# Kernel tuning notes

Measured on AMD Instinct MI355X. Metric: run time of the kernel, lower is better.

## Reference

```python
import jax, jax.numpy as jnp
import numpy as np


def setup_inputs() -> dict:
    key = jax.random.key(0)
    ks = jax.random.split(key, 4)
    T, B, I, H, L = 512, 64, 1024, 1024, 2
    s = 1.0 / np.sqrt(H)
    return {
        "x": jax.random.normal(ks[0], (T, B, I), dtype=jnp.float32),
        "W_ih": jax.random.uniform(ks[1], (L, 4 * H, I), dtype=jnp.float32, minval=-s, maxval=s),
        "W_hh": jax.random.uniform(ks[2], (L, 4 * H, H), dtype=jnp.float32, minval=-s, maxval=s),
        "b": jnp.zeros((L, 4 * H), dtype=jnp.float32),
        "h0": jnp.zeros((L, B, H), dtype=jnp.float32),
        "c0": jnp.zeros((L, B, H), dtype=jnp.float32),
    }


def _run_layer(xs, Wih, Whh, b, h0, c0):
    """xs: [T,B,I]; returns outputs [T,B,H], (h_T, c_T).
    Standard LSTM cell, PyTorch gate order (i, f, g, o)."""
    H = h0.shape[-1]

    # Precompute input projections for all timesteps in one big GEMM.
    gx = jnp.einsum("tbi,gi->tbg", xs, Wih) + b  # [T,B,4H]

    def step(carry, gx_t):
        h, c = carry
        g = gx_t + h @ Whh.T  # [B,4H]
        i = jax.nn.sigmoid(g[:, 0 * H:1 * H])
        f = jax.nn.sigmoid(g[:, 1 * H:2 * H])
        gg = jnp.tanh(g[:, 2 * H:3 * H])
        o = jax.nn.sigmoid(g[:, 3 * H:4 * H])
        c_next = f * c + i * gg
        h_next = o * jnp.tanh(c_next)
        return (h_next, c_next), h_next

    (h_n, c_n), out = jax.lax.scan(step, (h0, c0), gx)
    return out, h_n, c_n


def reference(x, W_ih, W_hh, b, h0, c0):
    """Eval-mode stacked LSTM (dropout=0, wdrop=0, gumbel noise p=0 -> identity).
    Returns (output [T,B,H], h_n [L,B,H], c_n [L,B,H])."""
    L = W_ih.shape[0]
    hs, cs = [], []
    layer_in = x
    for layer in range(L):
        layer_in, h_n, c_n = _run_layer(layer_in, W_ih[layer], W_hh[layer],
                                         b[layer], h0[layer], c0[layer])
        hs.append(h_n)
        cs.append(c_n)
    return layer_in, jnp.stack(hs, 0), jnp.stack(cs, 0)
```

## Files before the change

### kernel.cpp

```cpp
#include <hip/hip_runtime.h>

#define TT 512
#define BH 65536
#define NBLK 256

typedef unsigned short u16;
typedef __attribute__((ext_vector_type(8))) __bf16 bf16x8;
typedef __attribute__((ext_vector_type(4))) float f32x4;
typedef __attribute__((ext_vector_type(4))) float float4_t;
typedef __attribute__((ext_vector_type(2))) unsigned long long u64x2;

#define WS_XBF   0ull
#define WS_H1    67108864ull
#define WS_H2    (WS_H1 + 262144ull)
#define WS_FLAGS (WS_H2 + 262144ull)
#define WS_REL   (WS_FLAGS + 32768ull)

#define LDS_BYTES 132096

__device__ __forceinline__ u16 f2bf(float f) {
  unsigned u = __builtin_bit_cast(unsigned, f);
  u += 0x7fffu + ((u >> 16) & 1u);
  return (u16)(u >> 16);
}

__device__ __forceinline__ float sigm(float x) { return 1.0f / (1.0f + __expf(-x)); }
__device__ __forceinline__ float tanh_fast(float x) { return 1.0f - 2.0f / (__expf(2.0f * x) + 1.0f); }

__device__ __forceinline__ bf16x8 ld8_sc1(const u16* p) {
  u64x2 v;
  v.x = __hip_atomic_load((const unsigned long long*)p,       __ATOMIC_RELAXED, __HIP_MEMORY_SCOPE_AGENT);
  v.y = __hip_atomic_load((const unsigned long long*)(p + 4), __ATOMIC_RELAXED, __HIP_MEMORY_SCOPE_AGENT);
  return __builtin_bit_cast(bf16x8, v);
}

__global__ __launch_bounds__(256) void cast_x_kernel(const float* __restrict__ x, u16* __restrict__ xbf) {
  unsigned i = (blockIdx.x * 256u + threadIdx.x) * 4u;
  float4_t v = *(const float4_t*)(x + i);
  unsigned p0 = (unsigned)f2bf(v.x) | ((unsigned)f2bf(v.y) << 16);
  unsigned p1 = (unsigned)f2bf(v.z) | ((unsigned)f2bf(v.w) << 16);
  uint2 p; p.x = p0; p.y = p1;
  *(uint2*)(xbf + i) = p;
}

__global__ __launch_bounds__(256) void init_kernel(const float* __restrict__ h0,
                                                   u16* __restrict__ h1s, u16* __restrict__ h2s,
                                                   int* __restrict__ flags, int* __restrict__ rel) {
  unsigned idx = blockIdx.x * 256u + threadIdx.x;
  unsigned l = idx >> 16;
  unsigned pos = idx & 65535u;
  u16* dst = (l == 0 ? h1s : h2s) + BH + pos;
  *dst = f2bf(h0[idx]);
  if (idx < 8192) flags[idx] = 0;
  if (idx == 0) rel[0] = 0;
}

__global__ __launch_bounds__(256, 1) void lstm_kernel(
    const float* __restrict__ Wih, const float* __restrict__ Whh,
    const float* __restrict__ bias, const float* __restrict__ c0,
    const u16* __restrict__ xbf,
    u16* __restrict__ h1s, u16* __restrict__ h2s,
    float* __restrict__ out, int* __restrict__ flags, int* __restrict__ rel)
{
  extern __shared__ __align__(16) char smem_raw[];
  u16* lw = (u16*)smem_raw;
  const int tid = threadIdx.x;
  const int bid = blockIdx.x;
  const int layer = bid >> 7;
  const int lb = bid & 127;
  const int jbase = lb * 8;

  const float* WihL = Wih + (size_t)layer * 4096 * 1024;
  const float* WhhL = Whh + (size_t)layer * 4096 * 1024;
  for (int idx = tid; idx < 8192; idx += 256) {
    int n = idx >> 8;
    int k4 = (idx & 255) * 4;
    int gate = n >> 3, jj = n & 7;
    size_t grow = (size_t)(gate * 1024 + jbase + jj) * 1024 + k4;
    float4_t a = *(const float4_t*)(WihL + grow);
    float4_t b = *(const float4_t*)(WhhL + grow);
    u16* d0 = lw + n * 1032 + k4;
    u16* d1 = lw + 33024 + n * 1032 + k4;
    d0[0] = f2bf(a.x); d0[1] = f2bf(a.y); d0[2] = f2bf(a.z); d0[3] = f2bf(a.w);
    d1[0] = f2bf(b.x); d1[1] = f2bf(b.y); d1[2] = f2bf(b.z); d1[3] = f2bf(b.w);
  }

  const int lane = tid & 63;
  const int w = tid >> 6;
  const int q = lane >> 4;
  const int ln = lane & 15;
  const int arow = w * 16 + ln;
  const int koff = q * 8;
  const int jj = ln & 7;
  const bool act = ln < 8;
  const int col = jbase + jj;
  const int mrow0 = w * 16 + q * 4;

  const float* bL = bias + layer * 4096;
  const float bn0 = bL[(ln >> 3) * 1024 + jbase + jj];
  const float bn1 = bL[(2 + (ln >> 3)) * 1024 + jbase + jj];

  float c[4];
  {
    const float* c0L = c0 + (size_t)layer * BH;
#pragma unroll
    for (int r = 0; r < 4; ++r) c[r] = c0L[(mrow0 + r) * 1024 + col];
  }

  u16* mySlot = (layer == 0) ? h1s : h2s;
  const size_t OUT_HN = (size_t)TT * BH;
  const size_t OUT_CN = OUT_HN + 2 * BH;

  const u16* bW0 = lw + ln * 1032 + koff;
  const u16* bW1 = lw + (16 + ln) * 1032 + koff;
  const u16* bH0 = bW0 + 33024;
  const u16* bH1 = bW1 + 33024;

  __syncthreads();

  for (int it = 0; it <= TT; ++it) {
    const int t = (layer == 0) ? it : (it - 1);
    if (t >= 0 && t < TT) {
      const u16* a1p = mySlot + (size_t)((t - 1) & 1) * BH + arow * 1024 + koff;

      f32x4 acc0 = {0.f, 0.f, 0.f, 0.f};
      f32x4 acc1 = {0.f, 0.f, 0.f, 0.f};
      f32x4 acc2 = {0.f, 0.f, 0.f, 0.f};
      f32x4 acc3 = {0.f, 0.f, 0.f, 0.f};

      if (layer == 0) {
        const u16* a0p = xbf + (size_t)t * BH + arow * 1024 + koff;
#pragma unroll 16
        for (int kc = 0; kc < 32; ++kc) {
          bf16x8 a  = *(const bf16x8*)(a0p + kc * 32);
          bf16x8 b0 = *(const bf16x8*)(bW0 + kc * 32);
          bf16x8 b1 = *(const bf16x8*)(bW1 + kc * 32);
          if (kc & 1) {
            acc2 = __builtin_amdgcn_mfma_f32_16x16x32_bf16(a, b0, acc2, 0, 0, 0);
            acc3 = __builtin_amdgcn_mfma_f32_16x16x32_bf16(a, b1, acc3, 0, 0, 0);
          } else {
            acc0 = __builtin_amdgcn_mfma_f32_16x16x32_bf16(a, b0, acc0, 0, 0, 0);
            acc1 = __builtin_amdgcn_mfma_f32_16x16x32_bf16(a, b1, acc1, 0, 0, 0);
          }
        }
      } else {
        const u16* a0p = h1s + (size_t)(t & 1) * BH + arow * 1024 + koff;
#pragma unroll 16
        for (int kc = 0; kc < 32; ++kc) {
          bf16x8 a  = ld8_sc1(a0p + kc * 32);
          bf16x8 b0 = *(const bf16x8*)(bW0 + kc * 32);
          bf16x8 b1 = *(const bf16x8*)(bW1 + kc * 32);
          if (kc & 1) {
            acc2 = __builtin_amdgcn_mfma_f32_16x16x32_bf16(a, b0, acc2, 0, 0, 0);
            acc3 = __builtin_amdgcn_mfma_f32_16x16x32_bf16(a, b1, acc3, 0, 0, 0);
          } else {
            acc0 = __builtin_amdgcn_mfma_f32_16x16x32_bf16(a, b0, acc0, 0, 0, 0);
            acc1 = __builtin_amdgcn_mfma_f32_16x16x32_bf16(a, b1, acc1, 0, 0, 0);
          }
        }
      }
#pragma unroll 16
      for (int kc = 0; kc < 32; ++kc) {
        bf16x8 a  = ld8_sc1(a1p + kc * 32);
        bf16x8 b0 = *(const bf16x8*)(bH0 + kc * 32);
        bf16x8 b1 = *(const bf16x8*)(bH1 + kc * 32);
        if (kc & 1) {
          acc2 = __builtin_amdgcn_mfma_f32_16x16x32_bf16(a, b0, acc2, 0, 0, 0);
          acc3 = __builtin_amdgcn_mfma_f32_16x16x32_bf16(a, b1, acc3, 0, 0, 0);
        } else {
          acc0 = __builtin_amdgcn_mfma_f32_16x16x32_bf16(a, b0, acc0, 0, 0, 0);
          acc1 = __builtin_amdgcn_mfma_f32_16x16x32_bf16(a, b1, acc1, 0, 0, 0);
        }
      }

      float g0[4], g1[4], f4[4], o4[4];
#pragma unroll
      for (int r = 0; r < 4; ++r) { g0[r] = acc0[r] + acc2[r] + bn0; g1[r] = acc1[r] + acc3[r] + bn1; }
#pragma unroll
      for (int r = 0; r < 4; ++r) { f4[r] = __shfl_down(g0[r], 8); o4[r] = __shfl_down(g1[r], 8); }

      if (act) {
        float hn[4];
#pragma unroll
        for (int r = 0; r < 4; ++r) {
          float iv = sigm(g0[r]);
          float fv = sigm(f4[r]);
          float gv = tanh_fast(g1[r]);
          float ov = sigm(o4[r]);
          c[r] = fv * c[r] + iv * gv;
          hn[r] = ov * tanh_fast(c[r]);
        }
        u16* hdst = mySlot + (size_t)(t & 1) * BH;
#pragma unroll
        for (int r = 0; r < 4; ++r)
          __hip_atomic_store(&hdst[(mrow0 + r) * 1024 + col], f2bf(hn[r]),
                             __ATOMIC_RELAXED, __HIP_MEMORY_SCOPE_AGENT);
        if (layer == 1) {
          float* od = out + (size_t)t * BH;
#pragma unroll
          for (int r = 0; r < 4; ++r) od[(mrow0 + r) * 1024 + col] = hn[r];
        }
        if (t == TT - 1) {
#pragma unroll
          for (int r = 0; r < 4; ++r) {
            out[OUT_HN + (size_t)layer * BH + (mrow0 + r) * 1024 + col] = hn[r];
            out[OUT_CN + (size_t)layer * BH + (mrow0 + r) * 1024 + col] = c[r];
          }
        }
      }
    }

    if (it < TT) {
      __syncthreads();
      if (bid == 0) {
        if (tid > 0) {
          while (__hip_atomic_load(&flags[tid * 32], __ATOMIC_RELAXED,
                                   __HIP_MEMORY_SCOPE_AGENT) < it + 1)
            __builtin_amdgcn_s_sleep(1);
        }
        __syncthreads();
        if (tid == 0)
          __hip_atomic_store(rel, it + 1, __ATOMIC_RELAXED, __HIP_MEMORY_SCOPE_AGENT);
      } else {
        if (tid == 0) {
          __hip_atomic_store(&flags[bid * 32], it + 1, __ATOMIC_RELAXED,
                             __HIP_MEMORY_SCOPE_AGENT);
          while (__hip_atomic_load(rel, __ATOMIC_RELAXED,
                                   __HIP_MEMORY_SCOPE_AGENT) < it + 1)
            __builtin_amdgcn_s_sleep(1);
        }
        __syncthreads();
      }
      __builtin_amdgcn_fence(__ATOMIC_ACQUIRE, "workgroup");
    }
  }
}

extern "C" void kernel_launch(void* const* d_in, const int* in_sizes, int n_in,
                              void* d_out, int out_size, void* d_ws, size_t ws_size,
                              hipStream_t stream) {
  const float* x    = (const float*)d_in[0];
  const float* Wih  = (const float*)d_in[1];
  const float* Whh  = (const float*)d_in[2];
  const float* bias = (const float*)d_in[3];
  const float* h0   = (const float*)d_in[4];
  const float* c0   = (const float*)d_in[5];
  float* out = (float*)d_out;
  char* ws = (char*)d_ws;
  u16* xbf  = (u16*)(ws + WS_XBF);
  u16* h1s  = (u16*)(ws + WS_H1);
  u16* h2s  = (u16*)(ws + WS_H2);
  int* flags = (int*)(ws + WS_FLAGS);
  int* rel   = (int*)(ws + WS_REL);

  hipFuncSetAttribute((const void*)lstm_kernel,
                      hipFuncAttributeMaxDynamicSharedMemorySize, LDS_BYTES);

  cast_x_kernel<<<32768, 256, 0, stream>>>(x, xbf);
  init_kernel<<<512, 256, 0, stream>>>(h0, h1s, h2s, flags, rel);
  lstm_kernel<<<NBLK, 256, LDS_BYTES, stream>>>(Wih, Whh, bias, c0, xbf, h1s, h2s,
                                                out, flags, rel);
}
```

Before: 8.831 ms.

## Replace global barrier with per-block progress counters and a layer-1 ring buffer

Removes the centralized grid-wide barrier, in which block 0 gathered flags and released everyone each step. Each block now publishes a 16-bit progress counter, and one wavefront polls all 256 counters with packed 64-bit loads before each step. Layer 0's hidden states go into a 32-slot ring buffer, so layer 0 can run up to 31 steps ahead of layer 1 instead of moving in lockstep. Layer 0 also computes its input projection before waiting, which overlaps that work with synchronization. The cost is a larger workspace and heavier polling traffic on the counters.

```diff
diff --git a/kernel.cpp b/kernel.cpp
--- a/kernel.cpp
+++ b/kernel.cpp
@@ -2,7 +2,7 @@
 
 #define TT 512
 #define BH 65536
-#define NBLK 256
+#define NSLOT 32
 
 typedef unsigned short u16;
 typedef __attribute__((ext_vector_type(8))) __bf16 bf16x8;
@@ -11,10 +11,9 @@
 typedef __attribute__((ext_vector_type(2))) unsigned long long u64x2;
 
 #define WS_XBF   0ull
-#define WS_H1    67108864ull
-#define WS_H2    (WS_H1 + 262144ull)
-#define WS_FLAGS (WS_H2 + 262144ull)
-#define WS_REL   (WS_FLAGS + 32768ull)
+#define WS_H1R   67108864ull
+#define WS_H2    (WS_H1R + (unsigned long long)NSLOT * BH * 2)
+#define WS_CNT   (WS_H2 + 262144ull)
 
 #define LDS_BYTES 132096
 
@@ -44,23 +43,22 @@
 }
 
 __global__ __launch_bounds__(256) void init_kernel(const float* __restrict__ h0,
-                                                   u16* __restrict__ h1s, u16* __restrict__ h2s,
-                                                   int* __restrict__ flags, int* __restrict__ rel) {
+                                                   u16* __restrict__ h1r, u16* __restrict__ h2s,
+                                                   u16* __restrict__ cnt) {
   unsigned idx = blockIdx.x * 256u + threadIdx.x;
   unsigned l = idx >> 16;
   unsigned pos = idx & 65535u;
-  u16* dst = (l == 0 ? h1s : h2s) + BH + pos;
+  u16* dst = (l == 0 ? (h1r + (size_t)(NSLOT - 1) * BH) : (h2s + BH)) + pos;
   *dst = f2bf(h0[idx]);
-  if (idx < 8192) flags[idx] = 0;
-  if (idx == 0) rel[0] = 0;
+  if (idx < 256) cnt[idx] = 0;
 }
 
 __global__ __launch_bounds__(256, 1) void lstm_kernel(
     const float* __restrict__ Wih, const float* __restrict__ Whh,
     const float* __restrict__ bias, const float* __restrict__ c0,
     const u16* __restrict__ xbf,
-    u16* __restrict__ h1s, u16* __restrict__ h2s,
-    float* __restrict__ out, int* __restrict__ flags, int* __restrict__ rel)
+    u16* __restrict__ h1r, u16* __restrict__ h2s,
+    float* __restrict__ out, u16* __restrict__ cnt)
 {
   extern __shared__ __align__(16) char smem_raw[];
   u16* lw = (u16*)smem_raw;
@@ -107,7 +105,6 @@
     for (int r = 0; r < 4; ++r) c[r] = c0L[(mrow0 + r) * 1024 + col];
   }
 
-  u16* mySlot = (layer == 0) ? h1s : h2s;
   const size_t OUT_HN = (size_t)TT * BH;
   const size_t OUT_CN = OUT_HN + 2 * BH;
 
@@ -116,49 +113,53 @@
   const u16* bH0 = bW0 + 33024;
   const u16* bH1 = bW1 + 33024;
 
+  const int fragoff = arow * 1024 + koff;
+
   __syncthreads();
 
-  for (int it = 0; it <= TT; ++it) {
-    const int t = (layer == 0) ? it : (it - 1);
-    if (t >= 0 && t < TT) {
-      const u16* a1p = mySlot + (size_t)((t - 1) & 1) * BH + arow * 1024 + koff;
-
-      f32x4 acc0 = {0.f, 0.f, 0.f, 0.f};
-      f32x4 acc1 = {0.f, 0.f, 0.f, 0.f};
-      f32x4 acc2 = {0.f, 0.f, 0.f, 0.f};
-      f32x4 acc3 = {0.f, 0.f, 0.f, 0.f};
-
-      if (layer == 0) {
-        const u16* a0p = xbf + (size_t)t * BH + arow * 1024 + koff;
-#pragma unroll 16
-        for (int kc = 0; kc < 32; ++kc) {
-          bf16x8 a  = *(const bf16x8*)(a0p + kc * 32);
-          bf16x8 b0 = *(const bf16x8*)(bW0 + kc * 32);
-          bf16x8 b1 = *(const bf16x8*)(bW1 + kc * 32);
-          if (kc & 1) {
-            acc2 = __builtin_amdgcn_mfma_f32_16x16x32_bf16(a, b0, acc2, 0, 0, 0);
-            acc3 = __builtin_amdgcn_mfma_f32_16x16x32_bf16(a, b1, acc3, 0, 0, 0);
-          } else {
-            acc0 = __builtin_amdgcn_mfma_f32_16x16x32_bf16(a, b0, acc0, 0, 0, 0);
-            acc1 = __builtin_amdgcn_mfma_f32_16x16x32_bf16(a, b1, acc1, 0, 0, 0);
-          }
-        }
-      } else {
-        const u16* a0p = h1s + (size_t)(t & 1) * BH + arow * 1024 + koff;
-#pragma unroll 16
-        for (int kc = 0; kc < 32; ++kc) {
-          bf16x8 a  = ld8_sc1(a0p + kc * 32);
-          bf16x8 b0 = *(const bf16x8*)(bW0 + kc * 32);
-          bf16x8 b1 = *(const bf16x8*)(bW1 + kc * 32);
-          if (kc & 1) {
-            acc2 = __builtin_amdgcn_mfma_f32_16x16x32_bf16(a, b0, acc2, 0, 0, 0);
-            acc3 = __builtin_amdgcn_mfma_f32_16x16x32_bf16(a, b1, acc3, 0, 0, 0);
-          } else {
-            acc0 = __builtin_amdgcn_mfma_f32_16x16x32_bf16(a, b0, acc0, 0, 0, 0);
-            acc1 = __builtin_amdgcn_mfma_f32_16x16x32_bf16(a, b1, acc1, 0, 0, 0);
-          }
-        }
-      }
+  for (int t = 0; t < TT; ++t) {
+    f32x4 acc0 = {0.f, 0.f, 0.f, 0.f};
+    f32x4 acc1 = {0.f, 0.f, 0.f, 0.f};
+    f32x4 acc2 = {0.f, 0.f, 0.f, 0.f};
+    f32x4 acc3 = {0.f, 0.f, 0.f, 0.f};
+
+    if (layer == 0) {
+      const u16* a0p = xbf + (size_t)t * BH + fragoff;
+#pragma unroll 16
+      for (int kc = 0; kc < 32; ++kc) {
+        bf16x8 a  = *(const bf16x8*)(a0p + kc * 32);
+        bf16x8 b0 = *(const bf16x8*)(bW0 + kc * 32);
+        bf16x8 b1 = *(const bf16x8*)(bW1 + kc * 32);
+        if (kc & 1) {
+          acc2 = __builtin_amdgcn_mfma_f32_16x16x32_bf16(a, b0, acc2, 0, 0, 0);
+          acc3 = __builtin_amdgcn_mfma_f32_16x16x32_bf16(a, b1, acc3, 0, 0, 0);
+        } else {
+          acc0 = __builtin_amdgcn_mfma_f32_16x16x32_bf16(a, b0, acc0, 0, 0, 0);
+          acc1 = __builtin_amdgcn_mfma_f32_16x16x32_bf16(a, b1, acc1, 0, 0, 0);
+        }
+      }
+    }
+
+    if (tid < 64) {
+      const int tA = (layer == 0) ? t : t + 1;
+      int tB = (layer == 0) ? t - (NSLOT - 1) : t;
+      if (tB < 0) tB = 0;
+      const unsigned tgt = (unsigned)((tid < 32) ? tA : tB);
+      const unsigned long long* cp = (const unsigned long long*)(cnt + 4 * tid);
+      for (;;) {
+        unsigned long long v = __hip_atomic_load(cp, __ATOMIC_RELAXED, __HIP_MEMORY_SCOPE_AGENT);
+        int ok = ((unsigned)(v & 0xffffu) >= tgt) &
+                 ((unsigned)((v >> 16) & 0xffffu) >= tgt) &
+                 ((unsigned)((v >> 32) & 0xffffu) >= tgt) &
+                 ((unsigned)((v >> 48) & 0xffffu) >= tgt);
+        if (__all(ok)) break;
+        __builtin_amdgcn_s_sleep(4);
+      }
+    }
+    __syncthreads();
+
+    if (layer == 0) {
+      const u16* a1p = h1r + (size_t)((t + NSLOT - 1) & (NSLOT - 1)) * BH + fragoff;
 #pragma unroll 16
       for (int kc = 0; kc < 32; ++kc) {
         bf16x8 a  = ld8_sc1(a1p + kc * 32);
@@ -172,67 +173,77 @@
           acc1 = __builtin_amdgcn_mfma_f32_16x16x32_bf16(a, b1, acc1, 0, 0, 0);
         }
       }
-
-      float g0[4], g1[4], f4[4], o4[4];
-#pragma unroll
-      for (int r = 0; r < 4; ++r) { g0[r] = acc0[r] + acc2[r] + bn0; g1[r] = acc1[r] + acc3[r] + bn1; }
-#pragma unroll
-      for (int r = 0; r < 4; ++r) { f4[r] = __shfl_down(g0[r], 8); o4[r] = __shfl_down(g1[r], 8); }
-
-      if (act) {
-        float hn[4];
+    } else {
+      const u16* a0p = h1r + (size_t)(t & (NSLOT - 1)) * BH + fragoff;
+      const u16* a1p = h2s + (size_t)((t + 1) & 1) * BH + fragoff;
+#pragma unroll 16
+      for (int kc = 0; kc < 32; ++kc) {
+        bf16x8 a  = ld8_sc1(a0p + kc * 32);
+        bf16x8 b0 = *(const bf16x8*)(bW0 + kc * 32);
+        bf16x8 b1 = *(const bf16x8*)(bW1 + kc * 32);
+        if (kc & 1) {
+          acc2 = __builtin_amdgcn_mfma_f32_16x16x32_bf16(a, b0, acc2, 0, 0, 0);
+          acc3 = __builtin_amdgcn_mfma_f32_16x16x32_bf16(a, b1, acc3, 0, 0, 0);
+        } else {
+          acc0 = __builtin_amdgcn_mfma_f32_16x16x32_bf16(a, b0, acc0, 0, 0, 0);
+          acc1 = __builtin_amdgcn_mfma_f32_16x16x32_bf16(a, b1, acc1, 0, 0, 0);
+        }
+      }
+#pragma unroll 16
+      for (int kc = 0; kc < 32; ++kc) {
+        bf16x8 a  = ld8_sc1(a1p + kc * 32);
+        bf16x8 b0 = *(const bf16x8*)(bH0 + kc * 32);
+        bf16x8 b1 = *(const bf16x8*)(bH1 + kc * 32);
+        if (kc & 1) {
+          acc2 = __builtin_amdgcn_mfma_f32_16x16x32_bf16(a, b0, acc2, 0, 0, 0);
+          acc3 = __builtin_amdgcn_mfma_f32_16x16x32_bf16(a, b1, acc3, 0, 0, 0);
+        } else {
+          acc0 = __builtin_amdgcn_mfma_f32_16x16x32_bf16(a, b0, acc0, 0, 0, 0);
+          acc1 = __builtin_amdgcn_mfma_f32_16x16x32_bf16(a, b1, acc1, 0, 0, 0);
+        }
+      }
+    }
+
+    float g0[4], g1[4], f4[4], o4[4];
+#pragma unroll
+    for (int r = 0; r < 4; ++r) { g0[r] = acc0[r] + acc2[r] + bn0; g1[r] = acc1[r] + acc3[r] + bn1; }
+#pragma unroll
+    for (int r = 0; r < 4; ++r) { f4[r] = __shfl_down(g0[r], 8); o4[r] = __shfl_down(g1[r], 8); }
+
+    if (act) {
+      float hn[4];
+#pragma unroll
+      for (int r = 0; r < 4; ++r) {
+        float iv = sigm(g0[r]);
+        float fv = sigm(f4[r]);
+        float gv = tanh_fast(g1[r]);
+        float ov = sigm(o4[r]);
+        c[r] = fv * c[r] + iv * gv;
+        hn[r] = ov * tanh_fast(c[r]);
+      }
+      u16* hdst = (layer == 0) ? (h1r + (size_t)(t & (NSLOT - 1)) * BH)
+                               : (h2s + (size_t)(t & 1) * BH);
+#pragma unroll
+      for (int r = 0; r < 4; ++r)
+        __hip_atomic_store(&hdst[(mrow0 + r) * 1024 + col], f2bf(hn[r]),
+                           __ATOMIC_RELAXED, __HIP_MEMORY_SCOPE_AGENT);
+      if (layer == 1) {
+        float* od = out + (size_t)t * BH;
+#pragma unroll
+        for (int r = 0; r < 4; ++r) od[(mrow0 + r) * 1024 + col] = hn[r];
+      }
+      if (t == TT - 1) {
 #pragma unroll
         for (int r = 0; r < 4; ++r) {
-          float iv = sigm(g0[r]);
-          float fv = sigm(f4[r]);
-          float gv = tanh_fast(g1[r]);
-          float ov = sigm(o4[r]);
-          c[r] = fv * c[r] + iv * gv;
-          hn[r] = ov * tanh_fast(c[r]);
-        }
-        u16* hdst = mySlot + (size_t)(t & 1) * BH;
-#pragma unroll
-        for (int r = 0; r < 4; ++r)
-          __hip_atomic_store(&hdst[(mrow0 + r) * 1024 + col], f2bf(hn[r]),
-                             __ATOMIC_RELAXED, __HIP_MEMORY_SCOPE_AGENT);
-        if (layer == 1) {
-          float* od = out + (size_t)t * BH;
-#pragma unroll
-          for (int r = 0; r < 4; ++r) od[(mrow0 + r) * 1024 + col] = hn[r];
-        }
-        if (t == TT - 1) {
-#pragma unroll
-          for (int r = 0; r < 4; ++r) {
-            out[OUT_HN + (size_t)layer * BH + (mrow0 + r) * 1024 + col] = hn[r];
-            out[OUT_CN + (size_t)layer * BH + (mrow0 + r) * 1024 + col] = c[r];
-          }
-        }
-      }
-    }
-
-    if (it < TT) {
-      __syncthreads();
-      if (bid == 0) {
-        if (tid > 0) {
-          while (__hip_atomic_load(&flags[tid * 32], __ATOMIC_RELAXED,
-                                   __HIP_MEMORY_SCOPE_AGENT) < it + 1)
-            __builtin_amdgcn_s_sleep(1);
-        }
-        __syncthreads();
-        if (tid == 0)
-          __hip_atomic_store(rel, it + 1, __ATOMIC_RELAXED, __HIP_MEMORY_SCOPE_AGENT);
-      } else {
-        if (tid == 0) {
-          __hip_atomic_store(&flags[bid * 32], it + 1, __ATOMIC_RELAXED,
-                             __HIP_MEMORY_SCOPE_AGENT);
-          while (__hip_atomic_load(rel, __ATOMIC_RELAXED,
-                                   __HIP_MEMORY_SCOPE_AGENT) < it + 1)
-            __builtin_amdgcn_s_sleep(1);
-        }
-        __syncthreads();
-      }
-      __builtin_amdgcn_fence(__ATOMIC_ACQUIRE, "workgroup");
-    }
+          out[OUT_HN + (size_t)layer * BH + (mrow0 + r) * 1024 + col] = hn[r];
+          out[OUT_CN + (size_t)layer * BH + (mrow0 + r) * 1024 + col] = c[r];
+        }
+      }
+    }
+
+    __syncthreads();
+    if (tid == 0)
+      __hip_atomic_store(&cnt[bid], (u16)(t + 1), __ATOMIC_RELAXED, __HIP_MEMORY_SCOPE_AGENT);
   }
 }
 
@@ -247,17 +258,16 @@
   const float* c0   = (const float*)d_in[5];
   float* out = (float*)d_out;
   char* ws = (char*)d_ws;
-  u16* xbf  = (u16*)(ws + WS_XBF);
-  u16* h1s  = (u16*)(ws + WS_H1);
-  u16* h2s  = (u16*)(ws + WS_H2);
-  int* flags = (int*)(ws + WS_FLAGS);
-  int* rel   = (int*)(ws + WS_REL);
+  u16* xbf = (u16*)(ws + WS_XBF);
+  u16* h1r = (u16*)(ws + WS_H1R);
+  u16* h2s = (u16*)(ws + WS_H2);
+  u16* cnt = (u16*)(ws + WS_CNT);
 
   hipFuncSetAttribute((const void*)lstm_kernel,
                       hipFuncAttributeMaxDynamicSharedMemorySize, LDS_BYTES);
 
   cast_x_kernel<<<32768, 256, 0, stream>>>(x, xbf);
-  init_kernel<<<512, 256, 0, stream>>>(h0, h1s, h2s, flags, rel);
-  lstm_kernel<<<NBLK, 256, LDS_BYTES, stream>>>(Wih, Whh, bias, c0, xbf, h1s, h2s,
-                                                out, flags, rel);
-}
+  init_kernel<<<512, 256, 0, stream>>>(h0, h1r, h2s, cnt);
+  lstm_kernel<<<256, 256, LDS_BYTES, stream>>>(Wih, Whh, bias, c0, xbf, h1r, h2s,
+                                               out, cnt);
+}
```

Measured after the change: 9.715 ms. 10.0% more time.
